# Performance work log

Measured on AMD Instinct MI355X. Metric: run time of the kernel, lower is better.

The kernel has to match this reference:

```python
import jax, jax.numpy as jnp
import numpy as np

B, N, E = 2, 2048, 1024
H = 16
NE = 16                                  # num experts
TOPN = 2
CAP = max(4, int(N * 1.25 / NE))         # expert capacity = 160 (train, cf=1.25)
HFF = int(E * 4 * 2 / 3)                 # 2730, Expert_alt hidden
EPS = 1e-9
BLOCK = 64                               # spatial block size for block-causal mask


def setup_inputs():
    key = jax.random.key(0)
    ks = jax.random.split(key, 16)
    def nrm(k, shape, s=0.02):
        return jax.random.normal(k, shape, dtype=jnp.float32) * s
    # block-causal mask (tril over time blocks, repeat_interleave spatially); True = masked
    blk = np.tril(np.ones((N // BLOCK, N // BLOCK)))
    blk = np.repeat(np.repeat(blk, BLOCK, axis=0), BLOCK, axis=1)
    attn_mask = jnp.asarray(~blk.astype(bool))
    return dict(
        x=jax.random.normal(ks[0], (B, N, E), jnp.float32),
        attn_mask=attn_mask,
        in_proj_w=nrm(ks[1], (3 * E, E)),
        in_proj_b=jnp.zeros((3 * E,), jnp.float32),
        out_proj_w=nrm(ks[2], (E, E)),
        out_proj_b=jnp.zeros((E,), jnp.float32),
        rms_gamma=jnp.ones((E,), jnp.float32),
        gate_w=nrm(ks[3], (NE, E)),
        ln_g=jnp.ones((NE, E), jnp.float32),
        ln_b=jnp.zeros((NE, E), jnp.float32),
        w1=nrm(ks[4], (NE, HFF, E)),
        b1=jnp.zeros((NE, HFF), jnp.float32),
        w2=nrm(ks[5], (NE, E, HFF)),
        b2=jnp.zeros((NE, E), jnp.float32),
        route_unif=jax.random.uniform(ks[6], (TOPN, B, N), jnp.float32),
    )


def _layernorm(t, g, b, eps=1e-5):
    mu = t.mean(-1, keepdims=True)
    var = ((t - mu) ** 2).mean(-1, keepdims=True)
    return (t - mu) * jax.lax.rsqrt(var + eps) * g + b


def _forward(x, attn_mask, in_proj_w, in_proj_b, out_proj_w, out_proj_b,
             rms_gamma, gate_w, ln_g, ln_b, w1, b1, w2, b2, route_unif):
    dh = E // H
    # ---- multi-head self-attention (torch nn.MultiheadAttention math) ----
    qkv = x @ in_proj_w.T + in_proj_b                       # (B,N,3E)
    q, k, v = jnp.split(qkv, 3, axis=-1)
    to_heads = lambda t: t.reshape(B, N, H, dh).transpose(0, 2, 1, 3)
    q, k, v = to_heads(q), to_heads(k), to_heads(v)
    scores = jnp.einsum('bhqd,bhkd->bhqk', q, k) / jnp.sqrt(jnp.float32(dh))
    scores = jnp.where(attn_mask[None, None], -jnp.inf, scores)
    attn = jax.nn.softmax(scores, axis=-1)
    o = jnp.einsum('bhqk,bhkd->bhqd', attn, v).transpose(0, 2, 1, 3).reshape(B, N, E)
    o = o @ out_proj_w.T + out_proj_b
    y = o + x                                               # residual around MHA

    # ---- SparseMoEBlock: RMSNorm prenorm -> MoE -> residual ----
    residual = y
    nrm = y / jnp.clip(jnp.linalg.norm(y, axis=-1, keepdims=True), 1e-12)
    moe_in = nrm * jnp.sqrt(jnp.float32(E)) * rms_gamma

    # ---- top-2 gating (st-moe TopNGating, training mode) ----
    logits = moe_in @ gate_w.T                              # (B,N,NE)
    raw_gates = jax.nn.softmax(logits, axis=-1)
    gates_v, gate_idx = jax.lax.top_k(raw_gates, TOPN)      # (B,N,2)
    gates = jnp.moveaxis(gates_v, -1, 0)                    # (2,B,N)
    gate_idx = jnp.moveaxis(gate_idx, -1, 0)
    one_hot_idx = jax.nn.one_hot(gate_idx, NE, dtype=jnp.float32)  # (2,B,N,NE)
    mask = one_hot_idx
    mask_1 = mask[0]
    denom = jnp.clip(gates.sum(0, keepdims=True), EPS)
    gates = gates / denom
    threshold = jnp.array([EPS, 0.2], jnp.float32)[:, None, None]
    should_route = route_unif < gates / jnp.clip(threshold, EPS)
    should_route = should_route.at[0].set(True)             # always route to top-1
    mask = mask * should_route[..., None].astype(jnp.float32)
    mask_cumsum = jnp.cumsum(mask, axis=-2) - mask          # exclusive cumsum over N

    positions, masks_k = [], []
    prev = jnp.zeros((B, 1, NE), jnp.float32)
    capf = jnp.float32(CAP)
    for n_ in range(TOPN):
        pos = (mask_cumsum[n_] + prev) * mask[n_]           # (B,N,NE)
        mk = mask[n_] * (pos < capf).astype(jnp.float32)    # drop over-capacity
        prev = prev + mk.sum(axis=-2, keepdims=True)
        positions.append(pos.sum(-1))                       # (B,N)
        masks_k.append(mk)
    positions = jnp.stack(positions)                        # (2,B,N)
    mask = jnp.stack(masks_k)
    mask_flat = mask.sum(-1)                                # (2,B,N)
    gates = gates * mask_flat

    pos_oh = jax.nn.one_hot(positions.astype(jnp.int32), CAP, dtype=jnp.float32)  # (2,B,N,CAP)
    combine = jnp.einsum('kbn,kbn,kbne,kbnc->bnec', gates, mask_flat, one_hot_idx, pos_oh)
    dispatch_hard = (combine > 0).astype(jnp.float32)
    dispatch = dispatch_hard + combine - jax.lax.stop_gradient(combine)  # straight-through

    # ---- aux losses ----
    density_1 = mask_1.mean(-2)                             # (B,NE)
    density_proxy = raw_gates.mean(-2)
    balance_loss = (density_proxy * density_1).mean() * jnp.float32(NE ** 2)
    router_z_loss = jnp.mean(jax.nn.logsumexp(logits, axis=-1) ** 2)

    # ---- dispatch -> experts -> combine ----
    expert_inputs = jnp.einsum('bnd,bnec->ebcd', moe_in, dispatch)  # (NE,B,CAP,E)

    def expert_fn(g, bl, W1, B1, W2, B2, xin):
        h = _layernorm(xin, g, bl)
        h = h @ W1.T + B1
        h = jnp.where(h >= 0, h, 0.01 * h)                  # LeakyReLU(0.01)
        return h @ W2.T + B2

    expert_out = jax.vmap(expert_fn)(ln_g, ln_b, w1, b1, w2, b2, expert_inputs)
    moe_out = jnp.einsum('bnec,ebcd->bnd', combine, expert_out)

    out = moe_out + residual
    total_aux = balance_loss * 0.01 + router_z_loss * 0.001
    return out, total_aux, balance_loss, router_z_loss


def reference(x, attn_mask, in_proj_w, in_proj_b, out_proj_w, out_proj_b,
              rms_gamma, gate_w, ln_g, ln_b, w1, b1, w2, b2, route_unif):
    return _forward(x, attn_mask, in_proj_w, in_proj_b, out_proj_w, out_proj_b,
                    rms_gamma, gate_w, ln_g, ln_b, w1, b1, w2, b2, route_unif)
```

## Files before the change

### kernel.cpp

```cpp
#include <hip/hip_runtime.h>
#include <hip/hip_bf16.h>
#include <cstdint>

#define NSEQ  2048
#define BSZ   2
#define NTOK  4096
#define EDIM  1024
#define NEXP  16
#define CAPC  160
#define HFF_R 2730
#define HFF_P 2752

typedef __bf16 bf16_t;
typedef __bf16 bf16x8 __attribute__((ext_vector_type(8)));
typedef __bf16 bf16x4 __attribute__((ext_vector_type(4)));
typedef float  f32x4  __attribute__((ext_vector_type(4)));
typedef unsigned int uint32;

__device__ inline bf16x8 zero8() {
    bf16x8 v;
#pragma unroll
    for (int i = 0; i < 8; i++) v[i] = (bf16_t)0.f;
    return v;
}
__device__ inline bf16x8 pack8(float4 a, float4 b) {
    bf16x8 v;
    v[0]=(bf16_t)a.x; v[1]=(bf16_t)a.y; v[2]=(bf16_t)a.z; v[3]=(bf16_t)a.w;
    v[4]=(bf16_t)b.x; v[5]=(bf16_t)b.y; v[6]=(bf16_t)b.z; v[7]=(bf16_t)b.w;
    return v;
}
struct hl_t { bf16_t h, l; };
__device__ inline hl_t split1(float f) {
    hl_t r;
    r.h = (bf16_t)f;
    r.l = (bf16_t)(f - (float)r.h);
    return r;
}

template <int EPI, int C_SPLIT>
__global__ __launch_bounds__(256) void gemm_split(
    const float* __restrict__ A, const float* __restrict__ Bw,
    const float* __restrict__ bias, const float* __restrict__ resid,
    bf16_t* __restrict__ Chi, bf16_t* __restrict__ Clo, float* __restrict__ Cf,
    int M, int N, int K, int scale_cut, float scale_val)
{
    __shared__ __align__(16) bf16_t Ah[128 * 40], Al[128 * 40];
    __shared__ __align__(16) bf16_t Bh[128 * 40], Bl[128 * 40];
    const int t = threadIdx.x;
    const int m0 = blockIdx.y * 128, n0 = blockIdx.x * 128;
    const int lane = t & 63, l15 = lane & 15, lg = lane >> 4;
    const int wid = t >> 6, wm = wid >> 1, wn = wid & 1;
    const int srow = t >> 1, skc = (t & 1) * 16;

    f32x4 acc[4][4];
    const f32x4 zf = {0.f, 0.f, 0.f, 0.f};
#pragma unroll
    for (int i = 0; i < 4; i++)
#pragma unroll
        for (int j = 0; j < 4; j++) acc[i][j] = zf;

    float4 sa0, sa1, sa2, sa3, sb0, sb1, sb2, sb3;
    auto LOADAB = [&](int k0) {
        const float* ap = A + (long)(m0 + srow) * K + k0 + skc;
        sa0 = *(const float4*)ap;       sa1 = *(const float4*)(ap + 4);
        sa2 = *(const float4*)(ap + 8); sa3 = *(const float4*)(ap + 12);
        const float* bp = Bw + (long)(n0 + srow) * K + k0 + skc;
        sb0 = *(const float4*)bp;       sb1 = *(const float4*)(bp + 4);
        sb2 = *(const float4*)(bp + 8); sb3 = *(const float4*)(bp + 12);
    };
    auto WRITEAB = [&]() {
        float av[16], bv[16];
        *(float4*)&av[0] = sa0; *(float4*)&av[4] = sa1;
        *(float4*)&av[8] = sa2; *(float4*)&av[12] = sa3;
        *(float4*)&bv[0] = sb0; *(float4*)&bv[4] = sb1;
        *(float4*)&bv[8] = sb2; *(float4*)&bv[12] = sb3;
        bf16x8 h0, h1, l0, l1;
#pragma unroll
        for (int i = 0; i < 8; i++) {
            hl_t a = split1(av[i]);      h0[i] = a.h; l0[i] = a.l;
            hl_t b = split1(av[8 + i]);  h1[i] = b.h; l1[i] = b.l;
        }
        *(bf16x8*)&Ah[srow * 40 + skc] = h0; *(bf16x8*)&Ah[srow * 40 + skc + 8] = h1;
        *(bf16x8*)&Al[srow * 40 + skc] = l0; *(bf16x8*)&Al[srow * 40 + skc + 8] = l1;
#pragma unroll
        for (int i = 0; i < 8; i++) {
            hl_t a = split1(bv[i]);      h0[i] = a.h; l0[i] = a.l;
            hl_t b = split1(bv[8 + i]);  h1[i] = b.h; l1[i] = b.l;
        }
        *(bf16x8*)&Bh[srow * 40 + skc] = h0; *(bf16x8*)&Bh[srow * 40 + skc + 8] = h1;
        *(bf16x8*)&Bl[srow * 40 + skc] = l0; *(bf16x8*)&Bl[srow * 40 + skc + 8] = l1;
    };

    LOADAB(0);
    for (int k0 = 0; k0 < K; k0 += 32) {
        WRITEAB();
        __syncthreads();
        if (k0 + 32 < K) LOADAB(k0 + 32);
        bf16x8 amh[4], aml[4], bnh[4], bnl[4];
#pragma unroll
        for (int i = 0; i < 4; i++) {
            int base = (wm * 64 + i * 16 + l15) * 40 + lg * 8;
            amh[i] = *(const bf16x8*)&Ah[base];
            aml[i] = *(const bf16x8*)&Al[base];
        }
#pragma unroll
        for (int j = 0; j < 4; j++) {
            int base = (wn * 64 + j * 16 + l15) * 40 + lg * 8;
            bnh[j] = *(const bf16x8*)&Bh[base];
            bnl[j] = *(const bf16x8*)&Bl[base];
        }
#pragma unroll
        for (int i = 0; i < 4; i++)
#pragma unroll
            for (int j = 0; j < 4; j++) {
                acc[i][j] = __builtin_amdgcn_mfma_f32_16x16x32_bf16(amh[i], bnh[j], acc[i][j], 0, 0, 0);
                acc[i][j] = __builtin_amdgcn_mfma_f32_16x16x32_bf16(amh[i], bnl[j], acc[i][j], 0, 0, 0);
                acc[i][j] = __builtin_amdgcn_mfma_f32_16x16x32_bf16(aml[i], bnh[j], acc[i][j], 0, 0, 0);
            }
        __syncthreads();
    }

#pragma unroll
    for (int i = 0; i < 4; i++) {
        int mgb = m0 + wm * 64 + i * 16 + lg * 4;
#pragma unroll
        for (int j = 0; j < 4; j++) {
            int ng = n0 + wn * 64 + j * 16 + l15;
            float bval = bias[ng];
#pragma unroll
            for (int r = 0; r < 4; r++) {
                int mg = mgb + r;
                float val = acc[i][j][r] + bval;
                if (scale_cut > 0 && ng < scale_cut) val *= scale_val;
                if (EPI == 2) val += resid[(long)mg * N + ng];
                long idx = (long)mg * N + ng;
                if (C_SPLIT) {
                    bf16_t hi = (bf16_t)val;
                    Chi[idx] = hi;
                    Clo[idx] = (bf16_t)(val - (float)hi);
                } else {
                    Cf[idx] = val;
                }
            }
        }
    }
}

template <int EPI, int C_BF16, int BM>
__global__ __launch_bounds__(256) void gemm_nt(
    const bf16_t* __restrict__ Av, const float* __restrict__ Bw,
    const float* __restrict__ bias, void* __restrict__ Cv,
    int M, int N, int Nwr, int KA, int KB,
    long sAe, long sBe, long sBiasE, long sCe, int ldc)
{
    constexpr int MI = BM / 32;
    __shared__ __align__(16) bf16_t Alds[BM * 40];
    __shared__ __align__(16) bf16_t Blds[128 * 40];
    const int t = threadIdx.x;
    const int e = blockIdx.z;
    const int m0 = blockIdx.y * BM, n0 = blockIdx.x * 128;
    const int lane = t & 63, l15 = lane & 15, lg = lane >> 4;
    const int wid = t >> 6, wm = wid >> 1, wn = wid & 1;
    const int arow = (BM == 128) ? (t >> 1) : (t >> 2);
    const int acol = (BM == 128) ? ((t & 1) * 16) : ((t & 3) * 8);
    const int brow = t >> 1, bcol = (t & 1) * 16;

    f32x4 acc[MI][4];
    const f32x4 zf = {0.f, 0.f, 0.f, 0.f};
#pragma unroll
    for (int i = 0; i < MI; i++)
#pragma unroll
        for (int j = 0; j < 4; j++) acc[i][j] = zf;

    bf16x8 sa0, sa1;
    float4 sb0, sb1, sb2, sb3;
    const float4 zf4 = {0.f, 0.f, 0.f, 0.f};
    auto LOADA = [&](int k0) {
        int mg = m0 + arow;
        sa0 = zero8();
        if (BM == 128) sa1 = zero8();
        if (mg < M) {
            const bf16_t* ap = Av + (long)e * sAe + (long)mg * KA + k0 + acol;
            sa0 = *(const bf16x8*)ap;
            if (BM == 128) sa1 = *(const bf16x8*)(ap + 8);
        }
    };
    auto LOADB = [&](int k0) {
        int ng = n0 + brow;
        if (ng < N) {
            const float* bp = Bw + (long)e * sBe + (long)ng * KB + k0 + bcol;
            if (k0 + 32 <= KB) {
                sb0 = *(const float4*)bp;       sb1 = *(const float4*)(bp + 4);
                sb2 = *(const float4*)(bp + 8); sb3 = *(const float4*)(bp + 12);
            } else {
                float v[16];
#pragma unroll
                for (int i = 0; i < 16; i++) {
                    int kk = k0 + bcol + i;
                    v[i] = (kk < KB) ? bp[i] : 0.f;
                }
                sb0 = *(float4*)&v[0];  sb1 = *(float4*)&v[4];
                sb2 = *(float4*)&v[8];  sb3 = *(float4*)&v[12];
            }
        } else {
            sb0 = zf4; sb1 = zf4; sb2 = zf4; sb3 = zf4;
        }
    };
    auto WRITEAB = [&]() {
        *(bf16x8*)&Alds[arow * 40 + acol] = sa0;
        if (BM == 128) *(bf16x8*)&Alds[arow * 40 + acol + 8] = sa1;
        *(bf16x8*)&Blds[brow * 40 + bcol] = pack8(sb0, sb1);
        *(bf16x8*)&Blds[brow * 40 + bcol + 8] = pack8(sb2, sb3);
    };

    LOADA(0); LOADB(0);
    for (int k0 = 0; k0 < KA; k0 += 32) {
        WRITEAB();
        __syncthreads();
        if (k0 + 32 < KA) { LOADA(k0 + 32); LOADB(k0 + 32); }
        bf16x8 am[MI], bn[4];
#pragma unroll
        for (int i = 0; i < MI; i++)
            am[i] = *(const bf16x8*)&Alds[(wm * (BM / 2) + i * 16 + l15) * 40 + lg * 8];
#pragma unroll
        for (int j = 0; j < 4; j++)
            bn[j] = *(const bf16x8*)&Blds[(wn * 64 + j * 16 + l15) * 40 + lg * 8];
#pragma unroll
        for (int i = 0; i < MI; i++)
#pragma unroll
            for (int j = 0; j < 4; j++)
                acc[i][j] = __builtin_amdgcn_mfma_f32_16x16x32_bf16(am[i], bn[j], acc[i][j], 0, 0, 0);
        __syncthreads();
    }

    const float* biasp = bias + (long)e * sBiasE;
#pragma unroll
    for (int i = 0; i < MI; i++) {
        int mgb = m0 + wm * (BM / 2) + i * 16 + lg * 4;
#pragma unroll
        for (int j = 0; j < 4; j++) {
            int ng = n0 + wn * 64 + j * 16 + l15;
            if (ng < Nwr) {
                float bval = (ng < N) ? biasp[ng] : 0.f;
#pragma unroll
                for (int r = 0; r < 4; r++) {
                    int mg = mgb + r;
                    if (mg < M) {
                        float val = acc[i][j][r] + bval;
                        if (EPI == 1) val = (val >= 0.f) ? val : 0.01f * val;
                        if (ng >= N) val = 0.f;
                        long cidx = (long)e * sCe + (long)mg * ldc + ng;
                        if (C_BF16) ((bf16_t*)Cv)[cidx] = (bf16_t)val;
                        else        ((float*)Cv)[cidx] = val;
                    }
                }
            }
        }
    }
}

__global__ __launch_bounds__(256) void attn_split(const bf16_t* __restrict__ qh,
                                                  const bf16_t* __restrict__ ql,
                                                  float* __restrict__ o)
{
    __shared__ __align__(16) bf16_t KhS[64 * 72], KlS[64 * 72];
    __shared__ __align__(16) bf16_t VhS[64 * 72], VlS[64 * 72];
    __shared__ __align__(16) bf16_t PhS[4][2][16 * 72], PlS[4][2][16 * 72];

    const int id = blockIdx.x;
    const int x  = id & 7;
    const int s  = id >> 3;
    const int b  = s >> 5;
    const int s5 = s & 31;
    const int qraw = s5 & 15;
    const int h  = x + 8 * (s5 >> 4);
    const int qt = b ? (15 - qraw) : qraw;
    const int nkb = 2 * qt + 2;

    const int t = threadIdx.x, wid = t >> 6, lane = t & 63, l15 = lane & 15, lg = lane >> 4;
    const int krow = t >> 2, kdc = (t & 3) * 16;
    const int vk = t & 63, vdg = (t >> 6) * 16;
    const long kvb = (long)(b * NSEQ) * 3072 + 1024 + h * 64;
    const f32x4 zf = {0.f, 0.f, 0.f, 0.f};

    const long qo0 = (long)(b * NSEQ + qt * 128 + wid * 16 + l15) * 3072 + h * 64 + lg * 8;
    const long qo1 = qo0 + (long)64 * 3072;
    bf16x8 q0h0 = *(const bf16x8*)(qh + qo0), q0h1 = *(const bf16x8*)(qh + qo0 + 32);
    bf16x8 q0l0 = *(const bf16x8*)(ql + qo0), q0l1 = *(const bf16x8*)(ql + qo0 + 32);
    bf16x8 q1h0 = *(const bf16x8*)(qh + qo1), q1h1 = *(const bf16x8*)(qh + qo1 + 32);
    bf16x8 q1l0 = *(const bf16x8*)(ql + qo1), q1l1 = *(const bf16x8*)(ql + qo1 + 32);

    f32x4 O0[4], O1[4];
    float m0r[4], l0r[4], m1r[4], l1r[4];
#pragma unroll
    for (int r = 0; r < 4; r++) {
        O0[r] = zf; O1[r] = zf;
        m0r[r] = -1e30f; l0r[r] = 0.f; m1r[r] = -1e30f; l1r[r] = 0.f;
    }

    bf16x8 skh0, skh1, skl0, skl1, svh0, svh1, svl0, svl1;
    auto LOADKV = [&](int kb) {
        long ko = kvb + (long)(kb * 64 + krow) * 3072 + kdc;
        skh0 = *(const bf16x8*)(qh + ko); skh1 = *(const bf16x8*)(qh + ko + 8);
        skl0 = *(const bf16x8*)(ql + ko); skl1 = *(const bf16x8*)(ql + ko + 8);
        long vo = kvb + 1024 + (long)(kb * 64 + vk) * 3072 + vdg;
        svh0 = *(const bf16x8*)(qh + vo); svh1 = *(const bf16x8*)(qh + vo + 8);
        svl0 = *(const bf16x8*)(ql + vo); svl1 = *(const bf16x8*)(ql + vo + 8);
    };
    auto WRITEKV = [&]() {
        *(bf16x8*)&KhS[krow * 72 + kdc]     = skh0;
        *(bf16x8*)&KhS[krow * 72 + kdc + 8] = skh1;
        *(bf16x8*)&KlS[krow * 72 + kdc]     = skl0;
        *(bf16x8*)&KlS[krow * 72 + kdc + 8] = skl1;
#pragma unroll
        for (int i = 0; i < 8; i++) {
            VhS[(vdg + i) * 72 + vk]     = svh0[i];
            VhS[(vdg + 8 + i) * 72 + vk] = svh1[i];
            VlS[(vdg + i) * 72 + vk]     = svl0[i];
            VlS[(vdg + 8 + i) * 72 + vk] = svl1[i];
        }
    };

    LOADKV(0);
    for (int kb = 0; kb < nkb; kb++) {
        __syncthreads();
        WRITEKV();
        __syncthreads();
        if (kb + 1 < nkb) LOADKV(kb + 1);
        const bool g0a = (kb < nkb - 1);
        f32x4 s0[4], s1[4];
#pragma unroll
        for (int ks = 0; ks < 4; ks++) {
            int base = (ks * 16 + l15) * 72 + lg * 8;
            bf16x8 kh0 = *(const bf16x8*)&KhS[base];
            bf16x8 kh1 = *(const bf16x8*)&KhS[base + 32];
            bf16x8 kl0 = *(const bf16x8*)&KlS[base];
            bf16x8 kl1 = *(const bf16x8*)&KlS[base + 32];
            f32x4 a = zf;
            a = __builtin_amdgcn_mfma_f32_16x16x32_bf16(q1h0, kh0, a, 0, 0, 0);
            a = __builtin_amdgcn_mfma_f32_16x16x32_bf16(q1h1, kh1, a, 0, 0, 0);
            a = __builtin_amdgcn_mfma_f32_16x16x32_bf16(q1h0, kl0, a, 0, 0, 0);
            a = __builtin_amdgcn_mfma_f32_16x16x32_bf16(q1h1, kl1, a, 0, 0, 0);
            a = __builtin_amdgcn_mfma_f32_16x16x32_bf16(q1l0, kh0, a, 0, 0, 0);
            a = __builtin_amdgcn_mfma_f32_16x16x32_bf16(q1l1, kh1, a, 0, 0, 0);
            s1[ks] = a;
            f32x4 c = zf;
            if (g0a) {
                c = __builtin_amdgcn_mfma_f32_16x16x32_bf16(q0h0, kh0, c, 0, 0, 0);
                c = __builtin_amdgcn_mfma_f32_16x16x32_bf16(q0h1, kh1, c, 0, 0, 0);
                c = __builtin_amdgcn_mfma_f32_16x16x32_bf16(q0h0, kl0, c, 0, 0, 0);
                c = __builtin_amdgcn_mfma_f32_16x16x32_bf16(q0h1, kl1, c, 0, 0, 0);
                c = __builtin_amdgcn_mfma_f32_16x16x32_bf16(q0l0, kh0, c, 0, 0, 0);
                c = __builtin_amdgcn_mfma_f32_16x16x32_bf16(q0l1, kh1, c, 0, 0, 0);
            }
            s0[ks] = c;
        }
        {
            float alpha[4];
#pragma unroll
            for (int r = 0; r < 4; r++) {
                float mt = fmaxf(fmaxf(s1[0][r], s1[1][r]), fmaxf(s1[2][r], s1[3][r]));
#pragma unroll
                for (int m = 1; m < 16; m <<= 1) mt = fmaxf(mt, __shfl_xor(mt, m));
                float mn = fmaxf(m1r[r], mt);
                alpha[r] = __expf(m1r[r] - mn);
                m1r[r] = mn;
            }
            float ladd[4] = {0.f, 0.f, 0.f, 0.f};
#pragma unroll
            for (int ks = 0; ks < 4; ks++)
#pragma unroll
                for (int r = 0; r < 4; r++) {
                    float p = __expf(s1[ks][r] - m1r[r]);
                    s1[ks][r] = p;
                    ladd[r] += p;
                }
#pragma unroll
            for (int r = 0; r < 4; r++) {
#pragma unroll
                for (int m = 1; m < 16; m <<= 1) ladd[r] += __shfl_xor(ladd[r], m);
                l1r[r] = l1r[r] * alpha[r] + ladd[r];
            }
#pragma unroll
            for (int sb = 0; sb < 4; sb++)
#pragma unroll
                for (int r = 0; r < 4; r++) O1[sb][r] *= alpha[r];
            bf16_t* pwh = &PhS[wid][1][0];
            bf16_t* pwl = &PlS[wid][1][0];
#pragma unroll
            for (int ks = 0; ks < 4; ks++)
#pragma unroll
                for (int r = 0; r < 4; r++) {
                    hl_t pv = split1(s1[ks][r]);
                    pwh[(lg * 4 + r) * 72 + ks * 16 + l15] = pv.h;
                    pwl[(lg * 4 + r) * 72 + ks * 16 + l15] = pv.l;
                }
        }
        if (g0a) {
            float alpha[4];
#pragma unroll
            for (int r = 0; r < 4; r++) {
                float mt = fmaxf(fmaxf(s0[0][r], s0[1][r]), fmaxf(s0[2][r], s0[3][r]));
#pragma unroll
                for (int m = 1; m < 16; m <<= 1) mt = fmaxf(mt, __shfl_xor(mt, m));
                float mn = fmaxf(m0r[r], mt);
                alpha[r] = __expf(m0r[r] - mn);
                m0r[r] = mn;
            }
            float ladd[4] = {0.f, 0.f, 0.f, 0.f};
#pragma unroll
            for (int ks = 0; ks < 4; ks++)
#pragma unroll
                for (int r = 0; r < 4; r++) {
                    float p = __expf(s0[ks][r] - m0r[r]);
                    s0[ks][r] = p;
                    ladd[r] += p;
                }
#pragma unroll
            for (int r = 0; r < 4; r++) {
#pragma unroll
                for (int m = 1; m < 16; m <<= 1) ladd[r] += __shfl_xor(ladd[r], m);
                l0r[r] = l0r[r] * alpha[r] + ladd[r];
            }
#pragma unroll
            for (int sb = 0; sb < 4; sb++)
#pragma unroll
                for (int r = 0; r < 4; r++) O0[sb][r] *= alpha[r];
            bf16_t* pwh = &PhS[wid][0][0];
            bf16_t* pwl = &PlS[wid][0][0];
#pragma unroll
            for (int ks = 0; ks < 4; ks++)
#pragma unroll
                for (int r = 0; r < 4; r++) {
                    hl_t pv = split1(s0[ks][r]);
                    pwh[(lg * 4 + r) * 72 + ks * 16 + l15] = pv.h;
                    pwl[(lg * 4 + r) * 72 + ks * 16 + l15] = pv.l;
                }
        }
#pragma unroll
        for (int kst = 0; kst < 2; kst++) {
            bf16x8 pf1h = *(const bf16x8*)&PhS[wid][1][l15 * 72 + kst * 32 + lg * 8];
            bf16x8 pf1l = *(const bf16x8*)&PlS[wid][1][l15 * 72 + kst * 32 + lg * 8];
            bf16x8 pf0h, pf0l;
            if (g0a) {
                pf0h = *(const bf16x8*)&PhS[wid][0][l15 * 72 + kst * 32 + lg * 8];
                pf0l = *(const bf16x8*)&PlS[wid][0][l15 * 72 + kst * 32 + lg * 8];
            }
#pragma unroll
            for (int sb = 0; sb < 4; sb++) {
                int base = (sb * 16 + l15) * 72 + kst * 32 + lg * 8;
                bf16x8 vfh = *(const bf16x8*)&VhS[base];
                bf16x8 vfl = *(const bf16x8*)&VlS[base];
                O1[sb] = __builtin_amdgcn_mfma_f32_16x16x32_bf16(pf1h, vfh, O1[sb], 0, 0, 0);
                O1[sb] = __builtin_amdgcn_mfma_f32_16x16x32_bf16(pf1h, vfl, O1[sb], 0, 0, 0);
                O1[sb] = __builtin_amdgcn_mfma_f32_16x16x32_bf16(pf1l, vfh, O1[sb], 0, 0, 0);
                if (g0a) {
                    O0[sb] = __builtin_amdgcn_mfma_f32_16x16x32_bf16(pf0h, vfh, O0[sb], 0, 0, 0);
                    O0[sb] = __builtin_amdgcn_mfma_f32_16x16x32_bf16(pf0h, vfl, O0[sb], 0, 0, 0);
                    O0[sb] = __builtin_amdgcn_mfma_f32_16x16x32_bf16(pf0l, vfh, O0[sb], 0, 0, 0);
                }
            }
        }
    }
#pragma unroll
    for (int sb = 0; sb < 4; sb++)
#pragma unroll
        for (int r = 0; r < 4; r++) {
            int qg0 = qt * 128 + wid * 16 + lg * 4 + r;
            int col = h * 64 + sb * 16 + l15;
            o[(long)(b * NSEQ + qg0) * 1024 + col] = O0[sb][r] / l0r[r];
            o[(long)(b * NSEQ + qg0 + 64) * 1024 + col] = O1[sb][r] / l1r[r];
        }
}

__global__ __launch_bounds__(256) void rmsnorm_kernel(const float* __restrict__ y,
                                                      const float* __restrict__ gamma,
                                                      float* __restrict__ moe)
{
    long base = (long)blockIdx.x * 1024;
    float4 v = ((const float4*)(y + base))[threadIdx.x];
    float ss = v.x * v.x + v.y * v.y + v.z * v.z + v.w * v.w;
#pragma unroll
    for (int m = 32; m; m >>= 1) ss += __shfl_xor(ss, m);
    __shared__ float ls[4];
    if ((threadIdx.x & 63) == 0) ls[threadIdx.x >> 6] = ss;
    __syncthreads();
    float tot = ls[0] + ls[1] + ls[2] + ls[3];
    float sc = 32.0f / fmaxf(sqrtf(tot), 1e-12f);
    float4 g = ((const float4*)gamma)[threadIdx.x];
    float4 ov;
    ov.x = v.x * sc * g.x; ov.y = v.y * sc * g.y; ov.z = v.z * sc * g.z; ov.w = v.w * sc * g.w;
    ((float4*)(moe + base))[threadIdx.x] = ov;
}

__global__ __launch_bounds__(256) void gating_kernel(
    const float* __restrict__ moe, const float* __restrict__ gw,
    const float* __restrict__ runif, uint32* __restrict__ tokpack,
    float* __restrict__ tokg, float* __restrict__ acc)
{
    const int wid = threadIdx.x >> 6, lane = threadIdx.x & 63;
    const int tk = blockIdx.x * 4 + wid;
    const int b = tk >> 11, n = tk & 2047;
    float xv[16];
    const float4* xr4 = (const float4*)(moe + (long)tk * 1024 + lane * 16);
#pragma unroll
    for (int i = 0; i < 4; i++) {
        float4 v = xr4[i];
        xv[4 * i] = v.x; xv[4 * i + 1] = v.y; xv[4 * i + 2] = v.z; xv[4 * i + 3] = v.w;
    }
    float logit[16];
#pragma unroll
    for (int e = 0; e < 16; e++) {
        const float4* wr4 = (const float4*)(gw + e * 1024 + lane * 16);
        float p = 0.f;
#pragma unroll
        for (int i = 0; i < 4; i++) {
            float4 w = wr4[i];
            p = fmaf(xv[4 * i], w.x, p);     p = fmaf(xv[4 * i + 1], w.y, p);
            p = fmaf(xv[4 * i + 2], w.z, p); p = fmaf(xv[4 * i + 3], w.w, p);
        }
#pragma unroll
        for (int m = 1; m < 64; m <<= 1) p += __shfl_xor(p, m);
        logit[e] = p;
    }
    int e0 = 0; float t0 = logit[0];
#pragma unroll
    for (int e = 1; e < 16; e++) if (logit[e] > t0) { t0 = logit[e]; e0 = e; }
    int e1 = (e0 == 0) ? 1 : 0; float t1 = logit[e1];
#pragma unroll
    for (int e = 0; e < 16; e++) if (e != e0 && logit[e] > t1) { t1 = logit[e]; e1 = e; }
    float g0n = 1.f / (1.f + __expf(t1 - t0));
    float g1n = 1.f / (1.f + __expf(t0 - t1));
    int sr1 = (runif[(long)(BSZ + b) * NSEQ + n] < g1n / 0.2f) ? 1 : 0;
    float mx = t0, sum = 0.f, raw[16];
#pragma unroll
    for (int e = 0; e < 16; e++) { raw[e] = __expf(logit[e] - mx); sum += raw[e]; }
    float inv = 1.f / sum;
    float lse = mx + __logf(sum);
    if (lane == 0) {
        tokpack[tk] = (uint32)e0 | ((uint32)e1 << 4) | ((uint32)sr1 << 8);
        tokg[2 * tk] = g0n; tokg[2 * tk + 1] = g1n;
        atomicAdd(&acc[32 + b * 16 + e0], 1.0f);
        atomicAdd(&acc[64], lse * lse);
    }
    if (lane < 16) atomicAdd(&acc[b * 16 + lane], raw[lane] * inv);
}

__global__ __launch_bounds__(512) void scan_kernel(const uint32* __restrict__ tokpack,
                                                   uint32* __restrict__ r0,
                                                   uint32* __restrict__ r1,
                                                   int* __restrict__ prev)
{
    const int b = blockIdx.x, t = threadIdx.x;
    const int wv = t >> 6, lane = t & 63;
    uint32 toks[4];
    *(uint4*)toks = ((const uint4*)(tokpack + b * NSEQ))[t];

    uint32 c0[8], c1[8];
#pragma unroll
    for (int j = 0; j < 8; j++) { c0[j] = 0u; c1[j] = 0u; }
#pragma unroll
    for (int i = 0; i < 4; i++) {
        uint32 p = toks[i];
        uint32 e0 = p & 15, e1 = (p >> 4) & 15, sr1 = (p >> 8) & 1;
        uint32 inc0 = 1u << ((e0 & 1) * 16);
        uint32 inc1 = sr1 << ((e1 & 1) * 16);
#pragma unroll
        for (int j = 0; j < 8; j++) {
            c0[j] += ((e0 >> 1) == (uint32)j) ? inc0 : 0u;
            c1[j] += ((e1 >> 1) == (uint32)j) ? inc1 : 0u;
        }
    }
    uint32 i0[8], i1[8];
#pragma unroll
    for (int j = 0; j < 8; j++) { i0[j] = c0[j]; i1[j] = c1[j]; }
#pragma unroll
    for (int off = 1; off < 64; off <<= 1) {
#pragma unroll
        for (int j = 0; j < 8; j++) {
            uint32 u0 = __shfl_up(i0[j], off);
            uint32 u1 = __shfl_up(i1[j], off);
            if (lane >= off) { i0[j] += u0; i1[j] += u1; }
        }
    }
    __shared__ uint32 wsum0[8][8], wsum1[8][8];
    if (lane == 63) {
#pragma unroll
        for (int j = 0; j < 8; j++) { wsum0[wv][j] = i0[j]; wsum1[wv][j] = i1[j]; }
    }
    __syncthreads();
    uint32 b0[8], b1[8];
#pragma unroll
    for (int j = 0; j < 8; j++) {
        uint32 s0 = 0u, s1 = 0u;
#pragma unroll
        for (int w = 0; w < 8; w++) {
            s0 += (w < wv) ? wsum0[w][j] : 0u;
            s1 += (w < wv) ? wsum1[w][j] : 0u;
        }
        b0[j] = s0 + i0[j] - c0[j];
        b1[j] = s1 + i1[j] - c1[j];
    }
    if (t == 0) {
#pragma unroll
        for (int j = 0; j < 8; j++) {
            uint32 tot = 0u;
#pragma unroll
            for (int w = 0; w < 8; w++) tot += wsum0[w][j];
            int tlo = (int)(tot & 0xffffu), thi = (int)(tot >> 16);
            prev[b * 16 + 2 * j]     = tlo < CAPC ? tlo : CAPC;
            prev[b * 16 + 2 * j + 1] = thi < CAPC ? thi : CAPC;
        }
    }
    uint32* rr0 = r0 + b * NSEQ + t * 4;
    uint32* rr1 = r1 + b * NSEQ + t * 4;
#pragma unroll
    for (int i = 0; i < 4; i++) {
        uint32 p = toks[i];
        uint32 e0 = p & 15, e1 = (p >> 4) & 15, sr1 = (p >> 8) & 1;
        uint32 sh0 = (e0 & 1) * 16, sh1 = (e1 & 1) * 16;
        uint32 w0 = 0u, w1 = 0u;
#pragma unroll
        for (int j = 0; j < 8; j++) {
            w0 += ((e0 >> 1) == (uint32)j) ? b0[j] : 0u;
            w1 += ((e1 >> 1) == (uint32)j) ? b1[j] : 0u;
        }
        uint32 s0 = (w0 >> sh0) & 0xffffu;
        uint32 s1v = (w1 >> sh1) & 0xffffu;
        uint32 kept = (s0 < CAPC) ? 1u : 0u;
        rr0[i] = e0 | (kept << 4) | (s0 << 5);
        rr1[i] = e1 | (sr1 << 4) | (s1v << 5);
        uint32 inc0 = 1u << sh0;
        uint32 inc1 = sr1 << sh1;
#pragma unroll
        for (int j = 0; j < 8; j++) {
            b0[j] += ((e0 >> 1) == (uint32)j) ? inc0 : 0u;
            b1[j] += ((e1 >> 1) == (uint32)j) ? inc1 : 0u;
        }
    }
}

__global__ __launch_bounds__(256) void gather_kernel(
    const float* __restrict__ moe, const uint32* __restrict__ r0,
    const uint32* __restrict__ r1, const int* __restrict__ prev,
    float* __restrict__ ein)
{
    int tk = blockIdx.x, b = tk >> 11;
    float4 v = ((const float4*)(moe + (long)tk * 1024))[threadIdx.x];
    uint32 a = r0[tk];
    if ((a >> 4) & 1) {
        long row = ((long)(a & 15) * 2 + b) * CAPC + (int)(a >> 5);
        ((float4*)(ein + row * 1024))[threadIdx.x] = v;
    }
    uint32 c = r1[tk];
    {
        int e = c & 15, sr1 = (c >> 4) & 1;
        int slot = (int)(c >> 5) + prev[b * 16 + e];
        if (sr1 && slot < CAPC) {
            long row = ((long)e * 2 + b) * CAPC + slot;
            ((float4*)(ein + row * 1024))[threadIdx.x] = v;
        }
    }
}

__global__ __launch_bounds__(256) void expert_ln_kernel(
    const float* __restrict__ ein, const float* __restrict__ g,
    const float* __restrict__ bb, bf16_t* __restrict__ eout)
{
    int row = blockIdx.x, e = row / (BSZ * CAPC);
    long base = (long)row * 1024;
    float4 v = ((const float4*)(ein + base))[threadIdx.x];
    float s = v.x + v.y + v.z + v.w;
    float ss = v.x * v.x + v.y * v.y + v.z * v.z + v.w * v.w;
#pragma unroll
    for (int m = 32; m; m >>= 1) { s += __shfl_xor(s, m); ss += __shfl_xor(ss, m); }
    __shared__ float l1[4], l2[4];
    if ((threadIdx.x & 63) == 0) { l1[threadIdx.x >> 6] = s; l2[threadIdx.x >> 6] = ss; }
    __syncthreads();
    float st = l1[0] + l1[1] + l1[2] + l1[3];
    float sst = l2[0] + l2[1] + l2[2] + l2[3];
    float mu = st * (1.f / 1024.f);
    float var = sst * (1.f / 1024.f) - mu * mu;
    float rstd = rsqrtf(var + 1e-5f);
    int d = threadIdx.x * 4;
    float4 gg = *(const float4*)(g + e * 1024 + d);
    float4 bv = *(const float4*)(bb + e * 1024 + d);
    bf16x4 ov;
    ov[0] = (bf16_t)((v.x - mu) * rstd * gg.x + bv.x);
    ov[1] = (bf16_t)((v.y - mu) * rstd * gg.y + bv.y);
    ov[2] = (bf16_t)((v.z - mu) * rstd * gg.z + bv.z);
    ov[3] = (bf16_t)((v.w - mu) * rstd * gg.w + bv.w);
    *(bf16x4*)(eout + base + d) = ov;
}

__global__ __launch_bounds__(256) void combine_kernel(
    const float* __restrict__ y, const float* __restrict__ eout,
    const uint32* __restrict__ r0, const uint32* __restrict__ r1,
    const float* __restrict__ tokg, const int* __restrict__ prev,
    float* __restrict__ out)
{
    int tk = blockIdx.x, b = tk >> 11;
    uint32 a = r0[tk], c = r1[tk];
    int k0f = (a >> 4) & 1;
    float w0 = k0f ? tokg[2 * tk] : 0.f;
    long row0 = ((long)(a & 15) * 2 + b) * CAPC + (int)(a >> 5);
    int e1 = c & 15;
    int slot1 = (int)(c >> 5) + prev[b * 16 + e1];
    int k1f = (((c >> 4) & 1) && slot1 < CAPC) ? 1 : 0;
    float w1 = k1f ? tokg[2 * tk + 1] : 0.f;
    long row1 = ((long)e1 * 2 + b) * CAPC + slot1;
    int i = threadIdx.x;
    float4 vy = ((const float4*)(y + (long)tk * 1024))[i];
    float4 a0 = {0.f, 0.f, 0.f, 0.f}, a1 = {0.f, 0.f, 0.f, 0.f};
    if (k0f) a0 = ((const float4*)(eout + row0 * 1024))[i];
    if (k1f) a1 = ((const float4*)(eout + row1 * 1024))[i];
    float4 ov;
    ov.x = vy.x + w0 * a0.x + w1 * a1.x;
    ov.y = vy.y + w0 * a0.y + w1 * a1.y;
    ov.z = vy.z + w0 * a0.z + w1 * a1.z;
    ov.w = vy.w + w0 * a0.w + w1 * a1.w;
    ((float4*)(out + (long)tk * 1024))[i] = ov;
}

__global__ void zero_acc_kernel(float* acc)
{
    if (threadIdx.x < 65) acc[threadIdx.x] = 0.f;
}

__global__ void finalize_kernel(const float* __restrict__ acc, float* __restrict__ tail)
{
    int t = threadIdx.x;
    float v = (t < 32) ? acc[t] * acc[32 + t] : 0.f;
#pragma unroll
    for (int m = 1; m < 64; m <<= 1) v += __shfl_xor(v, m);
    if (t == 0) {
        float bal = v * (8.0f / (2048.f * 2048.f));
        float z = acc[64] / 4096.f;
        tail[0] = 0.01f * bal + 0.001f * z;
        tail[1] = bal;
        tail[2] = z;
    }
}

extern "C" void kernel_launch(void* const* d_in, const int* in_sizes, int n_in,
                              void* d_out, int out_size, void* d_ws, size_t ws_size,
                              hipStream_t stream)
{
    (void)in_sizes; (void)n_in; (void)out_size; (void)ws_size;
    const float* x     = (const float*)d_in[0];
    const float* in_w  = (const float*)d_in[2];
    const float* in_b  = (const float*)d_in[3];
    const float* out_w = (const float*)d_in[4];
    const float* out_b = (const float*)d_in[5];
    const float* rg    = (const float*)d_in[6];
    const float* gw    = (const float*)d_in[7];
    const float* lng   = (const float*)d_in[8];
    const float* lnb   = (const float*)d_in[9];
    const float* w1    = (const float*)d_in[10];
    const float* b1    = (const float*)d_in[11];
    const float* w2    = (const float*)d_in[12];
    const float* b2    = (const float*)d_in[13];
    const float* runif = (const float*)d_in[14];
    float* out = (float*)d_out;

    size_t off = 0;
    char* wsb = (char*)d_ws;
    auto take = [&](size_t bytes) -> char* {
        char* p = wsb + off;
        off += (bytes + 255) & ~(size_t)255;
        return p;
    };
    bf16_t* qkvh = (bf16_t*)take((size_t)NTOK * 3072 * 2);
    bf16_t* qkvl = (bf16_t*)take((size_t)NTOK * 3072 * 2);
    float*  obuf = (float*)take((size_t)NTOK * 1024 * 4);
    float*  ybuf = (float*)take((size_t)NTOK * 1024 * 4);
    float*  moe  = (float*)take((size_t)NTOK * 1024 * 4);
    bf16_t* eln  = (bf16_t*)take((size_t)NEXP * BSZ * CAPC * 1024 * 2);
    bf16_t* hbuf = (bf16_t*)take((size_t)NEXP * BSZ * CAPC * HFF_P * 2);
    uint32* tokpack = (uint32*)take(NTOK * 4);
    float*  tokg = (float*)take(NTOK * 8);
    uint32* r0   = (uint32*)take(NTOK * 4);
    uint32* r1   = (uint32*)take(NTOK * 4);
    int*    prev = (int*)take(128);
    float*  acc  = (float*)take(1024);
    float*  ein  = (float*)qkvl;
    float*  eoutv = (float*)qkvh;

    zero_acc_kernel<<<1, 128, 0, stream>>>(acc);

    gemm_split<0, 1><<<dim3(24, 32), 256, 0, stream>>>(
        x, in_w, in_b, nullptr, qkvh, qkvl, nullptr,
        NTOK, 3072, 1024, 1024, 0.125f);

    attn_split<<<dim3(512), 256, 0, stream>>>(qkvh, qkvl, obuf);

    gemm_split<2, 0><<<dim3(8, 32), 256, 0, stream>>>(
        obuf, out_w, out_b, x, nullptr, nullptr, ybuf,
        NTOK, 1024, 1024, 0, 1.0f);

    rmsnorm_kernel<<<NTOK, 256, 0, stream>>>(ybuf, rg, moe);
    gating_kernel<<<NTOK / 4, 256, 0, stream>>>(moe, gw, runif, tokpack, tokg, acc);
    scan_kernel<<<dim3(BSZ), 512, 0, stream>>>(tokpack, r0, r1, prev);
    gather_kernel<<<NTOK, 256, 0, stream>>>(moe, r0, r1, prev, ein);
    expert_ln_kernel<<<NEXP * BSZ * CAPC, 256, 0, stream>>>(ein, lng, lnb, eln);

    gemm_nt<1, 1, 64><<<dim3(22, 5, 16), 256, 0, stream>>>(
        eln, w1, b1, hbuf, 320, HFF_R, HFF_P, 1024, 1024,
        (long)320 * 1024, (long)HFF_R * 1024, HFF_R, (long)320 * HFF_P, HFF_P);

    gemm_nt<0, 0, 64><<<dim3(8, 5, 16), 256, 0, stream>>>(
        hbuf, w2, b2, eoutv, 320, 1024, 1024, HFF_P, HFF_R,
        (long)320 * HFF_P, (long)1024 * HFF_R, 1024, (long)320 * 1024, 1024);

    combine_kernel<<<NTOK, 256, 0, stream>>>(ybuf, eoutv, r0, r1, tokg, prev, out);
    finalize_kernel<<<1, 64, 0, stream>>>(acc, out + (size_t)NTOK * 1024);
}
```

Baseline: 670.7 us.

## Split-K the second expert GEMM with narrower tiles and raise MFMA wave priority

The second expert GEMM now uses 64-wide N tiles and a 2-way K split, so it launches four times as many workgroups. Each split writes partial sums to its own buffer, and the combine kernel adds the two partials. Separately, s_setprio brackets are wrapped around the MFMA loops in the split GEMM, the NT GEMM and the attention kernel so matrix-core issue gets priority. In exchange, the split costs an extra fp32 partial buffer plus more global writes and reads in combine.

```diff
diff --git a/kernel.cpp b/kernel.cpp
--- a/kernel.cpp
+++ b/kernel.cpp
@@ -109,6 +109,7 @@
             bnh[j] = *(const bf16x8*)&Bh[base];
             bnl[j] = *(const bf16x8*)&Bl[base];
         }
+        __builtin_amdgcn_s_setprio(1);
 #pragma unroll
         for (int i = 0; i < 4; i++)
 #pragma unroll
@@ -117,6 +118,7 @@
                 acc[i][j] = __builtin_amdgcn_mfma_f32_16x16x32_bf16(amh[i], bnl[j], acc[i][j], 0, 0, 0);
                 acc[i][j] = __builtin_amdgcn_mfma_f32_16x16x32_bf16(aml[i], bnh[j], acc[i][j], 0, 0, 0);
             }
+        __builtin_amdgcn_s_setprio(0);
         __syncthreads();
     }
 
@@ -146,31 +148,35 @@
     }
 }
 
-template <int EPI, int C_BF16, int BM>
+template <int EPI, int C_BF16, int BM, int BN, int KSPLIT>
 __global__ __launch_bounds__(256) void gemm_nt(
     const bf16_t* __restrict__ Av, const float* __restrict__ Bw,
     const float* __restrict__ bias, void* __restrict__ Cv,
     int M, int N, int Nwr, int KA, int KB,
-    long sAe, long sBe, long sBiasE, long sCe, int ldc)
+    long sAe, long sBe, long sBiasE, long sCe, int ldc, long sKs)
 {
     constexpr int MI = BM / 32;
+    constexpr int NJ = BN / 32;
     __shared__ __align__(16) bf16_t Alds[BM * 40];
-    __shared__ __align__(16) bf16_t Blds[128 * 40];
+    __shared__ __align__(16) bf16_t Blds[BN * 40];
     const int t = threadIdx.x;
     const int e = blockIdx.z;
-    const int m0 = blockIdx.y * BM, n0 = blockIdx.x * 128;
+    const int ks = (KSPLIT > 1) ? ((int)blockIdx.y % KSPLIT) : 0;
+    const int m0 = ((KSPLIT > 1) ? ((int)blockIdx.y / KSPLIT) : (int)blockIdx.y) * BM;
+    const int n0 = blockIdx.x * BN;
     const int lane = t & 63, l15 = lane & 15, lg = lane >> 4;
     const int wid = t >> 6, wm = wid >> 1, wn = wid & 1;
     const int arow = (BM == 128) ? (t >> 1) : (t >> 2);
     const int acol = (BM == 128) ? ((t & 1) * 16) : ((t & 3) * 8);
-    const int brow = t >> 1, bcol = (t & 1) * 16;
-
-    f32x4 acc[MI][4];
+    const int brow = (BN == 128) ? (t >> 1) : (t >> 2);
+    const int bcol = (BN == 128) ? ((t & 1) * 16) : ((t & 3) * 8);
+
+    f32x4 acc[MI][NJ];
     const f32x4 zf = {0.f, 0.f, 0.f, 0.f};
 #pragma unroll
     for (int i = 0; i < MI; i++)
 #pragma unroll
-        for (int j = 0; j < 4; j++) acc[i][j] = zf;
+        for (int j = 0; j < NJ; j++) acc[i][j] = zf;
 
     bf16x8 sa0, sa1;
     float4 sb0, sb1, sb2, sb3;
@@ -191,13 +197,16 @@
             const float* bp = Bw + (long)e * sBe + (long)ng * KB + k0 + bcol;
             if (k0 + 32 <= KB) {
                 sb0 = *(const float4*)bp;       sb1 = *(const float4*)(bp + 4);
-                sb2 = *(const float4*)(bp + 8); sb3 = *(const float4*)(bp + 12);
+                if (BN == 128) { sb2 = *(const float4*)(bp + 8); sb3 = *(const float4*)(bp + 12); }
             } else {
                 float v[16];
+                const int nload = (BN == 128) ? 16 : 8;
 #pragma unroll
                 for (int i = 0; i < 16; i++) {
-                    int kk = k0 + bcol + i;
-                    v[i] = (kk < KB) ? bp[i] : 0.f;
+                    if (i < nload) {
+                        int kk = k0 + bcol + i;
+                        v[i] = (kk < KB) ? bp[i] : 0.f;
+                    } else v[i] = 0.f;
                 }
                 sb0 = *(float4*)&v[0];  sb1 = *(float4*)&v[4];
                 sb2 = *(float4*)&v[8];  sb3 = *(float4*)&v[12];
@@ -210,26 +219,30 @@
         *(bf16x8*)&Alds[arow * 40 + acol] = sa0;
         if (BM == 128) *(bf16x8*)&Alds[arow * 40 + acol + 8] = sa1;
         *(bf16x8*)&Blds[brow * 40 + bcol] = pack8(sb0, sb1);
-        *(bf16x8*)&Blds[brow * 40 + bcol + 8] = pack8(sb2, sb3);
+        if (BN == 128) *(bf16x8*)&Blds[brow * 40 + bcol + 8] = pack8(sb2, sb3);
     };
 
-    LOADA(0); LOADB(0);
-    for (int k0 = 0; k0 < KA; k0 += 32) {
+    const int kbeg = ks * (KA / KSPLIT);
+    const int kend = kbeg + (KA / KSPLIT);
+    LOADA(kbeg); LOADB(kbeg);
+    for (int k0 = kbeg; k0 < kend; k0 += 32) {
         WRITEAB();
         __syncthreads();
-        if (k0 + 32 < KA) { LOADA(k0 + 32); LOADB(k0 + 32); }
-        bf16x8 am[MI], bn[4];
+        if (k0 + 32 < kend) { LOADA(k0 + 32); LOADB(k0 + 32); }
+        bf16x8 am[MI], bn[NJ];
 #pragma unroll
         for (int i = 0; i < MI; i++)
             am[i] = *(const bf16x8*)&Alds[(wm * (BM / 2) + i * 16 + l15) * 40 + lg * 8];
 #pragma unroll
-        for (int j = 0; j < 4; j++)
-            bn[j] = *(const bf16x8*)&Blds[(wn * 64 + j * 16 + l15) * 40 + lg * 8];
+        for (int j = 0; j < NJ; j++)
+            bn[j] = *(const bf16x8*)&Blds[(wn * (BN / 2) + j * 16 + l15) * 40 + lg * 8];
+        __builtin_amdgcn_s_setprio(1);
 #pragma unroll
         for (int i = 0; i < MI; i++)
 #pragma unroll
-            for (int j = 0; j < 4; j++)
+            for (int j = 0; j < NJ; j++)
                 acc[i][j] = __builtin_amdgcn_mfma_f32_16x16x32_bf16(am[i], bn[j], acc[i][j], 0, 0, 0);
+        __builtin_amdgcn_s_setprio(0);
         __syncthreads();
     }
 
@@ -238,10 +251,10 @@
     for (int i = 0; i < MI; i++) {
         int mgb = m0 + wm * (BM / 2) + i * 16 + lg * 4;
 #pragma unroll
-        for (int j = 0; j < 4; j++) {
-            int ng = n0 + wn * 64 + j * 16 + l15;
+        for (int j = 0; j < NJ; j++) {
+            int ng = n0 + wn * (BN / 2) + j * 16 + l15;
             if (ng < Nwr) {
-                float bval = (ng < N) ? biasp[ng] : 0.f;
+                float bval = (ks == 0 && ng < N) ? biasp[ng] : 0.f;
 #pragma unroll
                 for (int r = 0; r < 4; r++) {
                     int mg = mgb + r;
@@ -249,7 +262,7 @@
                         float val = acc[i][j][r] + bval;
                         if (EPI == 1) val = (val >= 0.f) ? val : 0.01f * val;
                         if (ng >= N) val = 0.f;
-                        long cidx = (long)e * sCe + (long)mg * ldc + ng;
+                        long cidx = (long)e * sCe + (long)mg * ldc + ng + (long)ks * sKs;
                         if (C_BF16) ((bf16_t*)Cv)[cidx] = (bf16_t)val;
                         else        ((float*)Cv)[cidx] = val;
                     }
@@ -329,6 +342,7 @@
         if (kb + 1 < nkb) LOADKV(kb + 1);
         const bool g0a = (kb < nkb - 1);
         f32x4 s0[4], s1[4];
+        __builtin_amdgcn_s_setprio(1);
 #pragma unroll
         for (int ks = 0; ks < 4; ks++) {
             int base = (ks * 16 + l15) * 72 + lg * 8;
@@ -355,6 +369,7 @@
             }
             s0[ks] = c;
         }
+        __builtin_amdgcn_s_setprio(0);
         {
             float alpha[4];
 #pragma unroll
@@ -437,6 +452,7 @@
                     pwl[(lg * 4 + r) * 72 + ks * 16 + l15] = pv.l;
                 }
         }
+        __builtin_amdgcn_s_setprio(1);
 #pragma unroll
         for (int kst = 0; kst < 2; kst++) {
             bf16x8 pf1h = *(const bf16x8*)&PhS[wid][1][l15 * 72 + kst * 32 + lg * 8];
@@ -461,6 +477,7 @@
                 }
             }
         }
+        __builtin_amdgcn_s_setprio(0);
     }
 #pragma unroll
     for (int sb = 0; sb < 4; sb++)
@@ -694,7 +711,8 @@
 }
 
 __global__ __launch_bounds__(256) void combine_kernel(
-    const float* __restrict__ y, const float* __restrict__ eout,
+    const float* __restrict__ y, const float* __restrict__ ep0,
+    const float* __restrict__ ep1,
     const uint32* __restrict__ r0, const uint32* __restrict__ r1,
     const float* __restrict__ tokg, const int* __restrict__ prev,
     float* __restrict__ out)
@@ -712,8 +730,16 @@
     int i = threadIdx.x;
     float4 vy = ((const float4*)(y + (long)tk * 1024))[i];
     float4 a0 = {0.f, 0.f, 0.f, 0.f}, a1 = {0.f, 0.f, 0.f, 0.f};
-    if (k0f) a0 = ((const float4*)(eout + row0 * 1024))[i];
-    if (k1f) a1 = ((const float4*)(eout + row1 * 1024))[i];
+    if (k0f) {
+        float4 p = ((const float4*)(ep0 + row0 * 1024))[i];
+        float4 q = ((const float4*)(ep1 + row0 * 1024))[i];
+        a0.x = p.x + q.x; a0.y = p.y + q.y; a0.z = p.z + q.z; a0.w = p.w + q.w;
+    }
+    if (k1f) {
+        float4 p = ((const float4*)(ep0 + row1 * 1024))[i];
+        float4 q = ((const float4*)(ep1 + row1 * 1024))[i];
+        a1.x = p.x + q.x; a1.y = p.y + q.y; a1.z = p.z + q.z; a1.w = p.w + q.w;
+    }
     float4 ov;
     ov.x = vy.x + w0 * a0.x + w1 * a1.x;
     ov.y = vy.y + w0 * a0.y + w1 * a1.y;
@@ -777,6 +803,7 @@
     float*  moe  = (float*)take((size_t)NTOK * 1024 * 4);
     bf16_t* eln  = (bf16_t*)take((size_t)NEXP * BSZ * CAPC * 1024 * 2);
     bf16_t* hbuf = (bf16_t*)take((size_t)NEXP * BSZ * CAPC * HFF_P * 2);
+    float*  ep1  = (float*)take((size_t)NEXP * BSZ * CAPC * 1024 * 4);
     uint32* tokpack = (uint32*)take(NTOK * 4);
     float*  tokg = (float*)take(NTOK * 8);
     uint32* r0   = (uint32*)take(NTOK * 4);
@@ -784,7 +811,9 @@
     int*    prev = (int*)take(128);
     float*  acc  = (float*)take(1024);
     float*  ein  = (float*)qkvl;
-    float*  eoutv = (float*)qkvh;
+    float*  ep0  = (float*)qkvh;
+
+    const long sKs = (long)(ep1 - ep0);
 
     zero_acc_kernel<<<1, 128, 0, stream>>>(acc);
 
@@ -804,14 +833,14 @@
     gather_kernel<<<NTOK, 256, 0, stream>>>(moe, r0, r1, prev, ein);
     expert_ln_kernel<<<NEXP * BSZ * CAPC, 256, 0, stream>>>(ein, lng, lnb, eln);
 
-    gemm_nt<1, 1, 64><<<dim3(22, 5, 16), 256, 0, stream>>>(
+    gemm_nt<1, 1, 64, 128, 1><<<dim3(22, 5, 16), 256, 0, stream>>>(
         eln, w1, b1, hbuf, 320, HFF_R, HFF_P, 1024, 1024,
-        (long)320 * 1024, (long)HFF_R * 1024, HFF_R, (long)320 * HFF_P, HFF_P);
-
-    gemm_nt<0, 0, 64><<<dim3(8, 5, 16), 256, 0, stream>>>(
-        hbuf, w2, b2, eoutv, 320, 1024, 1024, HFF_P, HFF_R,
-        (long)320 * HFF_P, (long)1024 * HFF_R, 1024, (long)320 * 1024, 1024);
-
-    combine_kernel<<<NTOK, 256, 0, stream>>>(ybuf, eoutv, r0, r1, tokg, prev, out);
+        (long)320 * 1024, (long)HFF_R * 1024, HFF_R, (long)320 * HFF_P, HFF_P, 0);
+
+    gemm_nt<0, 0, 64, 64, 2><<<dim3(16, 10, 16), 256, 0, stream>>>(
+        hbuf, w2, b2, ep0, 320, 1024, 1024, HFF_P, HFF_R,
+        (long)320 * HFF_P, (long)1024 * HFF_R, 1024, (long)320 * 1024, 1024, sKs);
+
+    combine_kernel<<<NTOK, 256, 0, stream>>>(ybuf, ep0, ep1, r0, r1, tokg, prev, out);
     finalize_kernel<<<1, 64, 0, stream>>>(acc, out + (size_t)NTOK * 1024);
 }
```

After: 704.9 us. 1.05x slower.

## Retile expert GEMMs to 64x64 with K=64 steps and raise MFMA wave priority

Applied to the files above, without the earlier changes.

The expert FFN GEMMs switch from 64x128 tiles with K-step 32 to 64x64 tiles with K-step 64. This doubles the grid (43x5x16 and 16x5x16) so more CUs are busy, and halves the number of barriers per K. Separately, s_setprio is raised around the MFMA sections in the split GEMM, the expert GEMM and both attention matmul phases, so waves issuing matrix ops get scheduling priority over load-issuing waves. The smaller tiles lower per-block data reuse, which means more global and LDS traffic for each FLOP.

```diff
diff --git a/kernel.cpp b/kernel.cpp
--- a/kernel.cpp
+++ b/kernel.cpp
@@ -109,6 +109,7 @@
             bnh[j] = *(const bf16x8*)&Bh[base];
             bnl[j] = *(const bf16x8*)&Bl[base];
         }
+        __builtin_amdgcn_s_setprio(1);
 #pragma unroll
         for (int i = 0; i < 4; i++)
 #pragma unroll
@@ -117,6 +118,7 @@
                 acc[i][j] = __builtin_amdgcn_mfma_f32_16x16x32_bf16(amh[i], bnl[j], acc[i][j], 0, 0, 0);
                 acc[i][j] = __builtin_amdgcn_mfma_f32_16x16x32_bf16(aml[i], bnh[j], acc[i][j], 0, 0, 0);
             }
+        __builtin_amdgcn_s_setprio(0);
         __syncthreads();
     }
 
@@ -146,57 +148,53 @@
     }
 }
 
-template <int EPI, int C_BF16, int BM>
-__global__ __launch_bounds__(256) void gemm_nt(
+template <int EPI, int C_BF16>
+__global__ __launch_bounds__(256) void gemm_nt64(
     const bf16_t* __restrict__ Av, const float* __restrict__ Bw,
     const float* __restrict__ bias, void* __restrict__ Cv,
     int M, int N, int Nwr, int KA, int KB,
     long sAe, long sBe, long sBiasE, long sCe, int ldc)
 {
-    constexpr int MI = BM / 32;
-    __shared__ __align__(16) bf16_t Alds[BM * 40];
-    __shared__ __align__(16) bf16_t Blds[128 * 40];
+    __shared__ __align__(16) bf16_t Alds[64 * 72];
+    __shared__ __align__(16) bf16_t Blds[64 * 72];
     const int t = threadIdx.x;
     const int e = blockIdx.z;
-    const int m0 = blockIdx.y * BM, n0 = blockIdx.x * 128;
+    const int m0 = blockIdx.y * 64, n0 = blockIdx.x * 64;
     const int lane = t & 63, l15 = lane & 15, lg = lane >> 4;
     const int wid = t >> 6, wm = wid >> 1, wn = wid & 1;
-    const int arow = (BM == 128) ? (t >> 1) : (t >> 2);
-    const int acol = (BM == 128) ? ((t & 1) * 16) : ((t & 3) * 8);
-    const int brow = t >> 1, bcol = (t & 1) * 16;
-
-    f32x4 acc[MI][4];
+    const int srow = t >> 2, scol = (t & 3) * 16;
+
+    f32x4 acc[2][2];
     const f32x4 zf = {0.f, 0.f, 0.f, 0.f};
 #pragma unroll
-    for (int i = 0; i < MI; i++)
-#pragma unroll
-        for (int j = 0; j < 4; j++) acc[i][j] = zf;
+    for (int i = 0; i < 2; i++)
+#pragma unroll
+        for (int j = 0; j < 2; j++) acc[i][j] = zf;
 
     bf16x8 sa0, sa1;
     float4 sb0, sb1, sb2, sb3;
     const float4 zf4 = {0.f, 0.f, 0.f, 0.f};
     auto LOADA = [&](int k0) {
-        int mg = m0 + arow;
-        sa0 = zero8();
-        if (BM == 128) sa1 = zero8();
+        int mg = m0 + srow;
+        sa0 = zero8(); sa1 = zero8();
         if (mg < M) {
-            const bf16_t* ap = Av + (long)e * sAe + (long)mg * KA + k0 + acol;
+            const bf16_t* ap = Av + (long)e * sAe + (long)mg * KA + k0 + scol;
             sa0 = *(const bf16x8*)ap;
-            if (BM == 128) sa1 = *(const bf16x8*)(ap + 8);
+            sa1 = *(const bf16x8*)(ap + 8);
         }
     };
     auto LOADB = [&](int k0) {
-        int ng = n0 + brow;
+        int ng = n0 + srow;
         if (ng < N) {
-            const float* bp = Bw + (long)e * sBe + (long)ng * KB + k0 + bcol;
-            if (k0 + 32 <= KB) {
+            const float* bp = Bw + (long)e * sBe + (long)ng * KB + k0 + scol;
+            if (k0 + 64 <= KB) {
                 sb0 = *(const float4*)bp;       sb1 = *(const float4*)(bp + 4);
                 sb2 = *(const float4*)(bp + 8); sb3 = *(const float4*)(bp + 12);
             } else {
                 float v[16];
 #pragma unroll
                 for (int i = 0; i < 16; i++) {
-                    int kk = k0 + bcol + i;
+                    int kk = k0 + scol + i;
                     v[i] = (kk < KB) ? bp[i] : 0.f;
                 }
                 sb0 = *(float4*)&v[0];  sb1 = *(float4*)&v[4];
@@ -207,39 +205,44 @@
         }
     };
     auto WRITEAB = [&]() {
-        *(bf16x8*)&Alds[arow * 40 + acol] = sa0;
-        if (BM == 128) *(bf16x8*)&Alds[arow * 40 + acol + 8] = sa1;
-        *(bf16x8*)&Blds[brow * 40 + bcol] = pack8(sb0, sb1);
-        *(bf16x8*)&Blds[brow * 40 + bcol + 8] = pack8(sb2, sb3);
+        *(bf16x8*)&Alds[srow * 72 + scol]     = sa0;
+        *(bf16x8*)&Alds[srow * 72 + scol + 8] = sa1;
+        *(bf16x8*)&Blds[srow * 72 + scol]     = pack8(sb0, sb1);
+        *(bf16x8*)&Blds[srow * 72 + scol + 8] = pack8(sb2, sb3);
     };
 
     LOADA(0); LOADB(0);
-    for (int k0 = 0; k0 < KA; k0 += 32) {
+    for (int k0 = 0; k0 < KA; k0 += 64) {
         WRITEAB();
         __syncthreads();
-        if (k0 + 32 < KA) { LOADA(k0 + 32); LOADB(k0 + 32); }
-        bf16x8 am[MI], bn[4];
-#pragma unroll
-        for (int i = 0; i < MI; i++)
-            am[i] = *(const bf16x8*)&Alds[(wm * (BM / 2) + i * 16 + l15) * 40 + lg * 8];
-#pragma unroll
-        for (int j = 0; j < 4; j++)
-            bn[j] = *(const bf16x8*)&Blds[(wn * 64 + j * 16 + l15) * 40 + lg * 8];
-#pragma unroll
-        for (int i = 0; i < MI; i++)
-#pragma unroll
-            for (int j = 0; j < 4; j++)
-                acc[i][j] = __builtin_amdgcn_mfma_f32_16x16x32_bf16(am[i], bn[j], acc[i][j], 0, 0, 0);
+        if (k0 + 64 < KA) { LOADA(k0 + 64); LOADB(k0 + 64); }
+#pragma unroll
+        for (int ks = 0; ks < 2; ks++) {
+            bf16x8 am[2], bn[2];
+#pragma unroll
+            for (int i = 0; i < 2; i++)
+                am[i] = *(const bf16x8*)&Alds[(wm * 32 + i * 16 + l15) * 72 + ks * 32 + lg * 8];
+#pragma unroll
+            for (int j = 0; j < 2; j++)
+                bn[j] = *(const bf16x8*)&Blds[(wn * 32 + j * 16 + l15) * 72 + ks * 32 + lg * 8];
+            __builtin_amdgcn_s_setprio(1);
+#pragma unroll
+            for (int i = 0; i < 2; i++)
+#pragma unroll
+                for (int j = 0; j < 2; j++)
+                    acc[i][j] = __builtin_amdgcn_mfma_f32_16x16x32_bf16(am[i], bn[j], acc[i][j], 0, 0, 0);
+            __builtin_amdgcn_s_setprio(0);
+        }
         __syncthreads();
     }
 
     const float* biasp = bias + (long)e * sBiasE;
 #pragma unroll
-    for (int i = 0; i < MI; i++) {
-        int mgb = m0 + wm * (BM / 2) + i * 16 + lg * 4;
-#pragma unroll
-        for (int j = 0; j < 4; j++) {
-            int ng = n0 + wn * 64 + j * 16 + l15;
+    for (int i = 0; i < 2; i++) {
+        int mgb = m0 + wm * 32 + i * 16 + lg * 4;
+#pragma unroll
+        for (int j = 0; j < 2; j++) {
+            int ng = n0 + wn * 32 + j * 16 + l15;
             if (ng < Nwr) {
                 float bval = (ng < N) ? biasp[ng] : 0.f;
 #pragma unroll
@@ -329,6 +332,7 @@
         if (kb + 1 < nkb) LOADKV(kb + 1);
         const bool g0a = (kb < nkb - 1);
         f32x4 s0[4], s1[4];
+        __builtin_amdgcn_s_setprio(1);
 #pragma unroll
         for (int ks = 0; ks < 4; ks++) {
             int base = (ks * 16 + l15) * 72 + lg * 8;
@@ -355,6 +359,7 @@
             }
             s0[ks] = c;
         }
+        __builtin_amdgcn_s_setprio(0);
         {
             float alpha[4];
 #pragma unroll
@@ -437,6 +442,7 @@
                     pwl[(lg * 4 + r) * 72 + ks * 16 + l15] = pv.l;
                 }
         }
+        __builtin_amdgcn_s_setprio(1);
 #pragma unroll
         for (int kst = 0; kst < 2; kst++) {
             bf16x8 pf1h = *(const bf16x8*)&PhS[wid][1][l15 * 72 + kst * 32 + lg * 8];
@@ -461,6 +467,7 @@
                 }
             }
         }
+        __builtin_amdgcn_s_setprio(0);
     }
 #pragma unroll
     for (int sb = 0; sb < 4; sb++)
@@ -804,11 +811,11 @@
     gather_kernel<<<NTOK, 256, 0, stream>>>(moe, r0, r1, prev, ein);
     expert_ln_kernel<<<NEXP * BSZ * CAPC, 256, 0, stream>>>(ein, lng, lnb, eln);
 
-    gemm_nt<1, 1, 64><<<dim3(22, 5, 16), 256, 0, stream>>>(
+    gemm_nt64<1, 1><<<dim3(43, 5, 16), 256, 0, stream>>>(
         eln, w1, b1, hbuf, 320, HFF_R, HFF_P, 1024, 1024,
         (long)320 * 1024, (long)HFF_R * 1024, HFF_R, (long)320 * HFF_P, HFF_P);
 
-    gemm_nt<0, 0, 64><<<dim3(8, 5, 16), 256, 0, stream>>>(
+    gemm_nt64<0, 0><<<dim3(16, 5, 16), 256, 0, stream>>>(
         hbuf, w2, b2, eoutv, 320, 1024, 1024, HFF_P, HFF_R,
         (long)320 * HFF_P, (long)1024 * HFF_R, 1024, (long)320 * 1024, 1024);
 
```

After: 687.9 us. 1.03x slower.
